# Performance work log

Measured on AMD Instinct MI355X. Metric: run time of the kernel, lower is better.

Reference implementation:

```python
import jax, jax.numpy as jnp
import numpy as np

# Static hyperparameters matching init_kwargs
G, N, D = 8, 8, 8          # groups, filters/group, kernel depth (c = G*D, o = G*N)
W, KS = 16, 4              # kernel width (time window), time stride
AH, AS = 2, 2              # activate_height, activate_stride (freq box-sum window)
C, F = 64, 128             # input channels, embedding (freq bins)
O = G * N                  # out_channels


def setup_inputs() -> dict:
    key = jax.random.key(0)
    kx, kw = jax.random.split(key)
    x = jax.random.normal(kx, (16, C, F, 256), dtype=jnp.float32)
    # xavier-uniform for weight (o, d, e, w)
    fan_in = D * F * W
    fan_out = fan_in  # torch xavier on 4D: fan computed over receptive field; bound below matches scale
    bound = float(np.sqrt(6.0 / (fan_in + fan_out)))
    weight = jax.random.uniform(kw, (O, D, F, W), dtype=jnp.float32, minval=-bound, maxval=bound)
    return {"x": x, "weight": weight}


def reference(x, weight):
    b, c, f, T = x.shape
    t = (T - W) // KS + 1
    # unfold time: x[..., ti*KS + wi] -> [b, c, f, t, W]
    idx = jnp.arange(t)[:, None] * KS + jnp.arange(W)[None, :]
    xu = x[..., idx]
    # split channels (g d) row-major, matching einops 'b (g d) f t w'
    xg = xu.reshape(b, G, D, f, t, W)
    wg = weight.reshape(G, N, D, f, W)
    # fused: multiply-broadcast then sum over d and w (the ones-kernel conv sums
    # over depth d and full width w); height window handled below.
    z = jnp.einsum('bgdftw,gndfw->btgnf', xg, wg)  # [b, t, G, N, f]
    z = z.reshape(b, t, O, f)
    # box-sum over freq with window AH, stride AS ('valid')
    fp = (f - AH) // AS + 1
    pidx = jnp.arange(fp)[:, None] * AS + jnp.arange(AH)
    y = z[..., pidx].sum(-1)  # [b, t, O, fp]
    return jnp.transpose(y, (0, 2, 3, 1))  # [b, O, fp, t]
```

## Files before the change

### kernel.cpp

```cpp
#include <hip/hip_runtime.h>


namespace {
constexpr int kC  = 64;
constexpr int kF  = 128;
constexpr int kT  = 256;
constexpr int kD  = 8;
constexpr int kN  = 8;
constexpr int kW  = 16;
constexpr int kKS = 4;
constexpr int kNT = 61;
constexpr int kO  = 64;
constexpr int kFP = 64;
constexpr int kQN = 4096;
constexpr int kQD = 512;
constexpr int kQF = 4;
}

__global__ __launch_bounds__(256, 8)
void lc2d_kernel(const float* __restrict__ x,
                 const float* __restrict__ wt,
                 float* __restrict__ out) {
  const int lane = threadIdx.x & 63;
  const int wv   = threadIdx.x >> 6;
  const int fi   = blockIdx.x;
  const int g    = blockIdx.y;
  const int b    = blockIdx.z * 4 + wv;

  const int tc   = (lane < kNT) ? lane : (kNT - 1);
  const int tau0 = tc * kKS;

  const float* xb =
      x + (((size_t)b * kC + g * kD) * kF + fi * 2) * kT + tau0;
  const float4* wb =
      (const float4*)(wt + ((size_t)(g * kN) * kD * kF + (size_t)fi * 2) * kW);

  float acc[kN];
#pragma unroll
  for (int n = 0; n < kN; ++n) acc[n] = 0.f;

#pragma unroll 2
  for (int it = 0; it < 16; ++it) {
    const int d  = it >> 1;
    const int fr = it & 1;

    const float* xr = xb + ((size_t)d * kF + fr) * kT;
    const float4 c0 = ((const float4*)xr)[0];
    const float4 c1 = ((const float4*)xr)[1];
    const float4 c2 = ((const float4*)xr)[2];
    const float4 c3 = ((const float4*)xr)[3];

    const float4* wit = wb + d * kQD + fr * kQF;

#pragma unroll
    for (int nb = 0; nb < 2; ++nb) {
      float4 w[16];
#pragma unroll
      for (int j = 0; j < 16; ++j)
        w[j] = wit[(size_t)(nb * 4 + (j >> 2)) * kQN + (j & 3)];
#pragma unroll
      for (int nn = 0; nn < 4; ++nn) {
        const float4 w0 = w[nn * 4 + 0];
        const float4 w1 = w[nn * 4 + 1];
        const float4 w2 = w[nn * 4 + 2];
        const float4 w3 = w[nn * 4 + 3];
        float a = acc[nb * 4 + nn];
        a = fmaf(c0.x, w0.x, a);
        a = fmaf(c0.y, w0.y, a);
        a = fmaf(c0.z, w0.z, a);
        a = fmaf(c0.w, w0.w, a);
        a = fmaf(c1.x, w1.x, a);
        a = fmaf(c1.y, w1.y, a);
        a = fmaf(c1.z, w1.z, a);
        a = fmaf(c1.w, w1.w, a);
        a = fmaf(c2.x, w2.x, a);
        a = fmaf(c2.y, w2.y, a);
        a = fmaf(c2.z, w2.z, a);
        a = fmaf(c2.w, w2.w, a);
        a = fmaf(c3.x, w3.x, a);
        a = fmaf(c3.y, w3.y, a);
        a = fmaf(c3.z, w3.z, a);
        a = fmaf(c3.w, w3.w, a);
        acc[nb * 4 + nn] = a;
      }
    }
  }

  if (lane < kNT) {
    const size_t s = (size_t)kFP * kNT;
    float* ob =
        out + (((size_t)b * kO + g * kN) * kFP + fi) * (size_t)kNT + lane;
#pragma unroll
    for (int n = 0; n < kN; ++n) ob[(size_t)n * s] = acc[n];
  }
}

extern "C" void kernel_launch(void* const* d_in, const int* in_sizes, int n_in,
                              void* d_out, int out_size, void* d_ws, size_t ws_size,
                              hipStream_t stream) {
  const float* x  = (const float*)d_in[0];
  const float* wt = (const float*)d_in[1];
  float* out      = (float*)d_out;

  dim3 grid(kFP, 8, 4);
  lc2d_kernel<<<grid, 256, 0, stream>>>(x, wt, out);
}
```

Before: 214.8 us.

## Remap lanes to (filter, depth) pairs with DPP reduction and streaming time window

Each lane now owns one output filter n and one depth index d, keeps its 32 weights in registers, and walks all 61 time steps sequentially. It streams x rows through a rotating register ring and reduces over depth with DPP cross-lane adds. This removes the repeated per-lane weight loads of the old layout, where every time-lane reloaded all weights, and makes x reads contiguous per lane. The costs are a fully unrolled 61-step loop, serial DPP reductions, stores from only one lane in eight, and lower occupancy bounds.

Result: slower. 302.9 us (+41.0%).

```diff
diff --git a/kernel.cpp b/kernel.cpp
--- a/kernel.cpp
+++ b/kernel.cpp
@@ -2,96 +2,86 @@
 
 
 namespace {
-constexpr int kC  = 64;
 constexpr int kF  = 128;
 constexpr int kT  = 256;
-constexpr int kD  = 8;
-constexpr int kN  = 8;
 constexpr int kW  = 16;
-constexpr int kKS = 4;
 constexpr int kNT = 61;
 constexpr int kO  = 64;
 constexpr int kFP = 64;
-constexpr int kQN = 4096;
-constexpr int kQD = 512;
-constexpr int kQF = 4;
 }
 
-__global__ __launch_bounds__(256, 8)
+typedef float f32x4 __attribute__((ext_vector_type(4)));
+
+__device__ __forceinline__ float dpp8_sum(float v) {
+  int r;
+  r = __builtin_amdgcn_update_dpp(0, __float_as_int(v), 0xB1, 0xF, 0xF, true);
+  v += __int_as_float(r);
+  r = __builtin_amdgcn_update_dpp(0, __float_as_int(v), 0x4E, 0xF, 0xF, true);
+  v += __int_as_float(r);
+  r = __builtin_amdgcn_update_dpp(0, __float_as_int(v), 0x141, 0xF, 0xF, true);
+  v += __int_as_float(r);
+  return v;
+}
+
+__global__ __launch_bounds__(256, 4)
 void lc2d_kernel(const float* __restrict__ x,
                  const float* __restrict__ wt,
                  float* __restrict__ out) {
   const int lane = threadIdx.x & 63;
   const int wv   = threadIdx.x >> 6;
+  const int n    = lane >> 3;
+  const int dq   = lane & 7;
   const int fi   = blockIdx.x;
   const int g    = blockIdx.y;
   const int b    = blockIdx.z * 4 + wv;
 
-  const int tc   = (lane < kNT) ? lane : (kNT - 1);
-  const int tau0 = tc * kKS;
+  const float* wb =
+      wt + (((size_t)((g * 8 + n) * 8 + dq)) * kF + 2 * fi) * kW;
+  f32x4 wq[2][4];
+#pragma unroll
+  for (int fr = 0; fr < 2; ++fr)
+#pragma unroll
+    for (int j = 0; j < 4; ++j)
+      wq[fr][j] = *(const f32x4*)(wb + fr * kW + 4 * j);
 
-  const float* xb =
-      x + (((size_t)b * kC + g * kD) * kF + fi * 2) * kT + tau0;
-  const float4* wb =
-      (const float4*)(wt + ((size_t)(g * kN) * kD * kF + (size_t)fi * 2) * kW);
+  const float* xr0 =
+      x + (((size_t)(b * 64 + g * 8 + dq)) * kF + 2 * fi) * kT;
+  const float* xr1 = xr0 + kT;
 
-  float acc[kN];
+  f32x4 q[2][8];
 #pragma unroll
-  for (int n = 0; n < kN; ++n) acc[n] = 0.f;
+  for (int j = 0; j < 6; ++j) {
+    q[0][j] = *(const f32x4*)(xr0 + 4 * j);
+    q[1][j] = *(const f32x4*)(xr1 + 4 * j);
+  }
 
-#pragma unroll 2
-  for (int it = 0; it < 16; ++it) {
-    const int d  = it >> 1;
-    const int fr = it & 1;
-
-    const float* xr = xb + ((size_t)d * kF + fr) * kT;
-    const float4 c0 = ((const float4*)xr)[0];
-    const float4 c1 = ((const float4*)xr)[1];
-    const float4 c2 = ((const float4*)xr)[2];
-    const float4 c3 = ((const float4*)xr)[3];
-
-    const float4* wit = wb + d * kQD + fr * kQF;
+  float* ob =
+      out + (((size_t)b * kO + g * 8 + n) * kFP + fi) * (size_t)kNT;
 
 #pragma unroll
-    for (int nb = 0; nb < 2; ++nb) {
-      float4 w[16];
+  for (int t = 0; t < kNT; ++t) {
+    float p0 = 0.f, p1 = 0.f;
 #pragma unroll
-      for (int j = 0; j < 16; ++j)
-        w[j] = wit[(size_t)(nb * 4 + (j >> 2)) * kQN + (j & 3)];
-#pragma unroll
-      for (int nn = 0; nn < 4; ++nn) {
-        const float4 w0 = w[nn * 4 + 0];
-        const float4 w1 = w[nn * 4 + 1];
-        const float4 w2 = w[nn * 4 + 2];
-        const float4 w3 = w[nn * 4 + 3];
-        float a = acc[nb * 4 + nn];
-        a = fmaf(c0.x, w0.x, a);
-        a = fmaf(c0.y, w0.y, a);
-        a = fmaf(c0.z, w0.z, a);
-        a = fmaf(c0.w, w0.w, a);
-        a = fmaf(c1.x, w1.x, a);
-        a = fmaf(c1.y, w1.y, a);
-        a = fmaf(c1.z, w1.z, a);
-        a = fmaf(c1.w, w1.w, a);
-        a = fmaf(c2.x, w2.x, a);
-        a = fmaf(c2.y, w2.y, a);
-        a = fmaf(c2.z, w2.z, a);
-        a = fmaf(c2.w, w2.w, a);
-        a = fmaf(c3.x, w3.x, a);
-        a = fmaf(c3.y, w3.y, a);
-        a = fmaf(c3.z, w3.z, a);
-        a = fmaf(c3.w, w3.w, a);
-        acc[nb * 4 + nn] = a;
-      }
+    for (int j = 0; j < 4; ++j) {
+      const f32x4 a0 = q[0][(t + j) & 7];
+      const f32x4 w0 = wq[0][j];
+      p0 = fmaf(a0.x, w0.x, p0);
+      p0 = fmaf(a0.y, w0.y, p0);
+      p0 = fmaf(a0.z, w0.z, p0);
+      p0 = fmaf(a0.w, w0.w, p0);
+      const f32x4 a1 = q[1][(t + j) & 7];
+      const f32x4 w1 = wq[1][j];
+      p1 = fmaf(a1.x, w1.x, p1);
+      p1 = fmaf(a1.y, w1.y, p1);
+      p1 = fmaf(a1.z, w1.z, p1);
+      p1 = fmaf(a1.w, w1.w, p1);
     }
-  }
-
-  if (lane < kNT) {
-    const size_t s = (size_t)kFP * kNT;
-    float* ob =
-        out + (((size_t)b * kO + g * kN) * kFP + fi) * (size_t)kNT + lane;
-#pragma unroll
-    for (int n = 0; n < kN; ++n) ob[(size_t)n * s] = acc[n];
+    const float p = dpp8_sum(p0 + p1);
+    if (dq == 0) ob[t] = p;
+    if (t <= 57) {
+      q[0][(t + 6) & 7] = *(const f32x4*)(xr0 + 4 * (t + 6));
+      q[1][(t + 6) & 7] = *(const f32x4*)(xr1 + 4 * (t + 6));
+    }
   }
 }
 
```
